# Kernel optimization log

Hardware: AMD Instinct MI355X
Metric: run time of the kernel (lower is better)

Reference implementation:

```python
import jax, jax.numpy as jnp
import numpy as np

DEPTH = 16
HID = 256
INP = 256
K = 2  # arity of the complete binary tree
TOTAL = (1 << (DEPTH + 1)) - 1  # 131071 nodes, level-order indexed


def setup_inputs() -> dict:
    key = jax.random.key(0)
    ks = jax.random.split(key, 14)
    s = 1.0 / np.sqrt(HID)
    inp = {
        "x": jax.random.normal(ks[0], (TOTAL, INP), jnp.float32),
        "Wi": jax.random.normal(ks[1], (HID, INP), jnp.float32) * s,
        "bi": jax.random.normal(ks[2], (HID,), jnp.float32) * s,
        "Wf": jax.random.normal(ks[3], (HID, INP), jnp.float32) * s,
        "bf": jax.random.normal(ks[4], (HID,), jnp.float32) * s,
        "Wo": jax.random.normal(ks[5], (HID, INP), jnp.float32) * s,
        "bo": jax.random.normal(ks[6], (HID,), jnp.float32) * s,
        "Wu": jax.random.normal(ks[7], (HID, INP), jnp.float32) * s,
        "bu": jax.random.normal(ks[8], (HID,), jnp.float32) * s,
        "Ui": jax.random.normal(ks[9], (HID, HID), jnp.float32) * s,
        "Uo": jax.random.normal(ks[10], (HID, HID), jnp.float32) * s,
        "Uu": jax.random.normal(ks[11], (HID, HID), jnp.float32) * s,
        "Wfk": jax.random.normal(ks[12], (K, HID, HID), jnp.float32) * s,
        "depth": DEPTH,
    }
    return inp


def reference(x, Wi, bi, Wf, bf, Wo, bo, Wu, bu, Ui, Uo, Uu, Wfk, depth):
    sig = jax.nn.sigmoid
    H = Ui.shape[0]
    # leaf level: leaf_forward (no recurrent terms)
    start, n = (1 << depth) - 1, 1 << depth
    xs = x[start:start + n]                      # [n, INP]
    i = sig(xs @ Wi.T + bi)
    o = sig(xs @ Wo.T + bo)
    u = jnp.tanh(xs @ Wu.T + bu)
    c = i * u
    h = o * jnp.tanh(c)
    # internal levels, bottom-up
    for d in range(depth - 1, -1, -1):
        start, n = (1 << d) - 1, 1 << d
        xs = x[start:start + n]                  # [n, INP]
        hc = h.reshape(n, K, H)                  # children h (level-order)
        cc = c.reshape(n, K, H)                  # children c
        Hs = hc.sum(axis=1)                      # sum over children, [n, H]
        i = sig(xs @ Wi.T + bi + Hs @ Ui.T)
        o = sig(xs @ Wo.T + bo + Hs @ Uo.T)
        u = jnp.tanh(xs @ Wu.T + bu + Hs @ Uu.T)
        # per-child-position forget gate; original applies wf{k} to the SUM of all children h
        fx = xs @ Wf.T + bf                      # [n, H]
        ukfh = jnp.einsum('ni,koi->nko', Hs, Wfk)  # [n, K, H]
        f = sig(fx[:, None, :] + ukfh)
        c = i * u + (f * cc).sum(axis=1)
        h = o * jnp.tanh(c)
    return jnp.stack([h, c])  # [2, 1, H]: root (h, c)
```

## Files before the change

### kernel.cpp

```cpp
#include <hip/hip_runtime.h>
#include <math.h>


#define LEAF_N 65536

typedef __attribute__((ext_vector_type(8))) short bf16x8;
typedef __attribute__((ext_vector_type(4))) float f32x4;

__device__ __forceinline__ float sigf(float x) { return 1.0f / (1.0f + expf(-x)); }

__device__ __forceinline__ unsigned short f2bf(float f) {
    union { float f; unsigned u; } v; v.f = f;
    unsigned r = v.u + 0x7fffu + ((v.u >> 16) & 1u);
    return (unsigned short)(r >> 16);
}

__host__ __device__ __forceinline__ size_t zoffD(int d) {
    return (d >= 4) ? (size_t)(65536 - (2 << d)) * 512
                    : (size_t)65536 * 512 + (size_t)(3 - d) * 8192;
}

__global__ __launch_bounds__(256) void pack_weights(
    const float* __restrict__ Wi, const float* __restrict__ bi,
    const float* __restrict__ Wf, const float* __restrict__ bf,
    const float* __restrict__ Wo, const float* __restrict__ bo,
    const float* __restrict__ Wu, const float* __restrict__ bu,
    const float* __restrict__ Ui, const float* __restrict__ Uo,
    const float* __restrict__ Uu, const float* __restrict__ Wfk,
    unsigned short* __restrict__ Wpk, unsigned short* __restrict__ WpkL,
    float* __restrict__ bbig, float* __restrict__ bleaf)
{
    int idx = blockIdx.x * 256 + threadIdx.x;
    const int NWB = 1280 * 512;
    const int NWL = 768 * 256;
    if (idx < NWB) {
        int j = idx & 7, l = (idx >> 3) & 63, kc = (idx >> 9) & 15, nt = idx >> 13;
        int row = nt * 16 + (l & 15);
        int k = kc * 32 + ((l >> 4) << 3) + j;
        int g = row >> 8, rr = row & 255;
        float v;
        if (k < 256) {
            const float* W = (g == 0) ? Wi : (g == 1) ? Wo : (g == 2) ? Wu : Wf;
            v = W[rr * 256 + k];
        } else {
            int kk = k - 256;
            v = (g == 0) ? Ui[rr * 256 + kk]
              : (g == 1) ? Uo[rr * 256 + kk]
              : (g == 2) ? Uu[rr * 256 + kk]
              : (g == 3) ? Wfk[rr * 256 + kk]
                         : Wfk[65536 + rr * 256 + kk];
        }
        Wpk[idx] = f2bf(v);
    } else if (idx < NWB + NWL) {
        int q = idx - NWB;
        int j = q & 7, l = (q >> 3) & 63, kc = (q >> 9) & 7, nt = q >> 12;
        int row = nt * 16 + (l & 15);
        int k = kc * 32 + ((l >> 4) << 3) + j;
        int g = row >> 8, rr = row & 255;
        const float* W = (g == 0) ? Wi : (g == 1) ? Wo : Wu;
        WpkL[q] = f2bf(W[rr * 256 + k]);
    } else if (idx < NWB + NWL + 1280) {
        int r = idx - NWB - NWL;
        int g = r >> 8, rr = r & 255;
        bbig[r] = (g == 0) ? bi[rr] : (g == 1) ? bo[rr] : (g == 2) ? bu[rr] : bf[rr];
    } else if (idx < NWB + NWL + 1280 + 768) {
        int r = idx - NWB - NWL - 1280;
        int g = r >> 8, rr = r & 255;
        bleaf[r] = (g == 0) ? bi[rr] : (g == 1) ? bo[rr] : bu[rr];
    }
}

__global__ __launch_bounds__(256) void cvt_all(
    const float* __restrict__ x, unsigned short* __restrict__ Zbuf,
    unsigned short* __restrict__ Xpk)
{
    int idx = blockIdx.x * 256 + threadIdx.x;
    if (idx >= 131071 * 32) return;
    int row = idx >> 5, k8 = idx & 31;
    const float* s = x + (size_t)row * 256 + k8 * 8;
    unsigned short r[8];
#pragma unroll
    for (int i = 0; i < 8; i++) r[i] = f2bf(s[i]);
    int kc = k8 >> 2;
    if (row < 65535) {
        int d = 31 - __clz(row + 1);
        int jn = row - ((1 << d) - 1);
        int l = (jn & 15) + ((k8 & 3) << 4);
        size_t dst = zoffD(d) + ((size_t)((jn >> 4) * 16 + kc) * 64 + l) * 8;
        *(uint4*)(Zbuf + dst) = *(uint4*)r;
    } else {
        int jn = row - 65535;
        int l = (jn & 15) + ((k8 & 3) << 4);
        size_t dst = ((size_t)((jn >> 4) * 8 + kc) * 64 + l) * 8;
        *(uint4*)(Xpk + dst) = *(uint4*)r;
    }
}

template<int NG, int KCN>
__global__ __launch_bounds__(512, 2) void fused_level(
    const unsigned short* __restrict__ Zpk, const unsigned short* __restrict__ Wpk,
    const float* __restrict__ bias, const float* __restrict__ csrc,
    float* __restrict__ c_out, unsigned short* __restrict__ zparent,
    int leaf_flag)
{
    const int tid = threadIdx.x, wave = tid >> 6, lane = tid & 63;
    const int bm = blockIdx.x * 32;
    const int cc = lane & 15, rq = (lane >> 4) * 4;

    f32x4 acc[2][2 * NG] = {};

    const unsigned short* aB = Zpk + ((size_t)(bm >> 4) * KCN * 64 + lane) * 8;
    const unsigned short* bB = Wpk + ((size_t)(2 * wave) * KCN * 64 + lane) * 8;

    bf16x8 afX[2], bvX[2 * NG];
    bf16x8 afY[2], bvY[2 * NG];

#pragma unroll
    for (int i = 0; i < 2; ++i)
        afX[i] = *(const bf16x8*)(aB + (size_t)(i * KCN) * 512);
#pragma unroll
    for (int g = 0; g < NG; ++g)
#pragma unroll
        for (int t = 0; t < 2; ++t)
            bvX[g * 2 + t] = *(const bf16x8*)(bB + (size_t)((g * 16 + t) * KCN) * 512);

    auto do_mfma = [&](bf16x8 (&af)[2], bf16x8 (&bv)[2 * NG]) {
#pragma unroll
        for (int g = 0; g < NG; ++g)
#pragma unroll
            for (int t = 0; t < 2; ++t)
#pragma unroll
                for (int i = 0; i < 2; ++i)
                    acc[i][g * 2 + t] = __builtin_amdgcn_mfma_f32_16x16x32_bf16(
                        af[i], bv[g * 2 + t], acc[i][g * 2 + t], 0, 0, 0);
    };

#pragma unroll
    for (int kc = 0; kc < KCN; kc += 2) {
#pragma unroll
        for (int i = 0; i < 2; ++i)
            afY[i] = *(const bf16x8*)(aB + (size_t)(i * KCN + kc + 1) * 512);
#pragma unroll
        for (int g = 0; g < NG; ++g)
#pragma unroll
            for (int t = 0; t < 2; ++t)
                bvY[g * 2 + t] = *(const bf16x8*)(bB + (size_t)((g * 16 + t) * KCN + kc + 1) * 512);
        do_mfma(afX, bvX);
        if (kc + 2 < KCN) {
#pragma unroll
            for (int i = 0; i < 2; ++i)
                afX[i] = *(const bf16x8*)(aB + (size_t)(i * KCN + kc + 2) * 512);
#pragma unroll
            for (int g = 0; g < NG; ++g)
#pragma unroll
                for (int t = 0; t < 2; ++t)
                    bvX[g * 2 + t] = *(const bf16x8*)(bB + (size_t)((g * 16 + t) * KCN + kc + 2) * 512);
        }
        do_mfma(afY, bvY);
    }

#pragma unroll
    for (int t = 0; t < 2; ++t) {
        const int h = (2 * wave + t) * 16 + cc;
        const float bI = bias[h], bO = bias[256 + h], bU = bias[512 + h];
        float bF0 = 0.f, bF1 = 0.f;
        if constexpr (NG == 5) { bF0 = bias[768 + h]; bF1 = bias[1024 + h]; }
#pragma unroll
        for (int mt = 0; mt < 2; ++mt) {
            const int node0 = bm + mt * 16 + rq;
            float hv[4];
#pragma unroll
            for (int r = 0; r < 4; ++r) {
                const int node = node0 + r;
                float iv = sigf(acc[mt][0 + t][r] + bI);
                float ov = sigf(acc[mt][2 + t][r] + bO);
                float uv = tanhf(acc[mt][4 + t][r] + bU);
                float cv = iv * uv;
                if constexpr (NG == 5) {
                    float f0 = sigf(acc[mt][6 + t][r] + bF0);
                    float f1 = sigf(acc[mt][8 + t][r] + bF1);
                    cv += f0 * csrc[(size_t)(2 * node) * 256 + h]
                        + f1 * csrc[(size_t)(2 * node + 1) * 256 + h];
                }
                c_out[(size_t)node * 256 + h] = cv;
                hv[r] = ov * tanhf(cv);
            }
#pragma unroll
            for (int pr = 0; pr < 2; ++pr) {
                const int p = ((node0 + 2 * pr) >> 1);
                size_t a = ((size_t)((p >> 4) * 16 + 8 + (h >> 5)) * 64
                            + (p & 15) + (((h >> 3) & 3) << 4)) * 8 + (h & 7);
                zparent[a] = f2bf(hv[2 * pr] + hv[2 * pr + 1]);
            }
        }
    }
    (void)leaf_flag;
}

__global__ __launch_bounds__(64) void small_gemm(
    const unsigned short* __restrict__ Zpk, const unsigned short* __restrict__ Wpk,
    const float* __restrict__ bias, float* __restrict__ pre, int n)
{
    const int lane = threadIdx.x;
    const int q = blockIdx.x;
    const int nt0 = (q >> 2) * 16 + (q & 3) * 4;
    const int cc = lane & 15, rq = (lane >> 4) * 4;

    f32x4 acc[4] = {};
    const unsigned short* aB = Zpk + (size_t)lane * 8;
    const unsigned short* bB = Wpk + ((size_t)nt0 * 16 * 64 + lane) * 8;

    bf16x8 aX, bX[4], aY, bY[4];
    aX = *(const bf16x8*)(aB);
#pragma unroll
    for (int j = 0; j < 4; ++j)
        bX[j] = *(const bf16x8*)(bB + (size_t)(j * 16) * 512);

#pragma unroll
    for (int kc = 0; kc < 16; kc += 2) {
        aY = *(const bf16x8*)(aB + (size_t)(kc + 1) * 512);
#pragma unroll
        for (int j = 0; j < 4; ++j)
            bY[j] = *(const bf16x8*)(bB + (size_t)(j * 16 + kc + 1) * 512);
#pragma unroll
        for (int j = 0; j < 4; ++j)
            acc[j] = __builtin_amdgcn_mfma_f32_16x16x32_bf16(aX, bX[j], acc[j], 0, 0, 0);
        if (kc + 2 < 16) {
            aX = *(const bf16x8*)(aB + (size_t)(kc + 2) * 512);
#pragma unroll
            for (int j = 0; j < 4; ++j)
                bX[j] = *(const bf16x8*)(bB + (size_t)(j * 16 + kc + 2) * 512);
        }
#pragma unroll
        for (int j = 0; j < 4; ++j)
            acc[j] = __builtin_amdgcn_mfma_f32_16x16x32_bf16(aY, bY[j], acc[j], 0, 0, 0);
    }

#pragma unroll
    for (int j = 0; j < 4; ++j) {
        int coln = (nt0 + j) * 16 + cc;
        float bb = bias[coln];
#pragma unroll
        for (int r = 0; r < 4; ++r) {
            int row = rq + r;
            if (row < n) pre[(size_t)row * 1280 + coln] = acc[j][r] + bb;
        }
    }
}

__global__ __launch_bounds__(256) void epi_small(
    const float* __restrict__ pre, const float* __restrict__ csrc,
    float* __restrict__ c_out, unsigned short* __restrict__ zparent,
    float* __restrict__ root_out, int npairs)
{
    int idx = blockIdx.x * 256 + threadIdx.x;
    if (root_out) {
        int h = idx;
        const float* p = pre;
        float c = sigf(p[h]) * tanhf(p[512 + h])
                + sigf(p[768 + h]) * csrc[h]
                + sigf(p[1024 + h]) * csrc[256 + h];
        root_out[h] = sigf(p[256 + h]) * tanhf(c);
        root_out[256 + h] = c;
        return;
    }
    if (idx >= npairs * 256) return;
    int pI = idx >> 8, h = idx & 255;
    int n0 = 2 * pI;
    const float* p0 = pre + (size_t)n0 * 1280;
    const float* p1 = p0 + 1280;
    float c0 = sigf(p0[h]) * tanhf(p0[512 + h])
             + sigf(p0[768 + h]) * csrc[(size_t)(2 * n0) * 256 + h]
             + sigf(p0[1024 + h]) * csrc[(size_t)(2 * n0 + 1) * 256 + h];
    float c1 = sigf(p1[h]) * tanhf(p1[512 + h])
             + sigf(p1[768 + h]) * csrc[(size_t)(2 * n0 + 2) * 256 + h]
             + sigf(p1[1024 + h]) * csrc[(size_t)(2 * n0 + 3) * 256 + h];
    float h0 = sigf(p0[256 + h]) * tanhf(c0);
    float h1 = sigf(p1[256 + h]) * tanhf(c1);
    c_out[(size_t)n0 * 256 + h] = c0;
    c_out[(size_t)(n0 + 1) * 256 + h] = c1;
    size_t a = ((size_t)((pI >> 4) * 16 + 8 + (h >> 5)) * 64
                + (pI & 15) + (((h >> 3) & 3) << 4)) * 8 + (h & 7);
    zparent[a] = f2bf(h0 + h1);
}

extern "C" void kernel_launch(void* const* d_in, const int* in_sizes, int n_in,
                              void* d_out, int out_size, void* d_ws, size_t ws_size,
                              hipStream_t stream)
{
    const float* x   = (const float*)d_in[0];
    const float* Wi  = (const float*)d_in[1];
    const float* bi  = (const float*)d_in[2];
    const float* Wf  = (const float*)d_in[3];
    const float* bf  = (const float*)d_in[4];
    const float* Wo  = (const float*)d_in[5];
    const float* bo  = (const float*)d_in[6];
    const float* Wu  = (const float*)d_in[7];
    const float* bu  = (const float*)d_in[8];
    const float* Ui  = (const float*)d_in[9];
    const float* Uo  = (const float*)d_in[10];
    const float* Uu  = (const float*)d_in[11];
    const float* Wfk = (const float*)d_in[12];
    float* out = (float*)d_out;
    char* ws   = (char*)d_ws;
    (void)ws_size; (void)in_sizes; (void)n_in; (void)out_size;

    size_t off = 0;
    unsigned short* Wpk  = (unsigned short*)(ws + off); off += (size_t)1280 * 512 * 2;
    unsigned short* WpkL = (unsigned short*)(ws + off); off += (size_t)768 * 256 * 2;
    float* bbig  = (float*)(ws + off); off += 1280 * 4;
    float* bleaf = (float*)(ws + off); off += 768 * 4 + 192;
    unsigned short* Xpk  = (unsigned short*)(ws + off); off += (size_t)65536 * 256 * 2;
    unsigned short* Zbuf = (unsigned short*)(ws + off); off += ((size_t)65536 * 512 + 32768) * 2;
    float* cA = (float*)(ws + off); off += (size_t)65536 * 256 * 4;
    float* cB = (float*)(ws + off); off += (size_t)32768 * 256 * 4;
    float* pre_small = (float*)(ws + off); off += (size_t)16 * 1280 * 4;

    pack_weights<<<3336, 256, 0, stream>>>(Wi, bi, Wf, bf, Wo, bo, Wu, bu,
                                           Ui, Uo, Uu, Wfk, Wpk, WpkL, bbig, bleaf);
    cvt_all<<<16385, 256, 0, stream>>>(x, Zbuf, Xpk);

    fused_level<3, 8><<<LEAF_N / 32, 512, 0, stream>>>(
        Xpk, WpkL, bleaf, nullptr, cA, Zbuf + zoffD(15), 1);

    for (int d = 15; d >= 5; d--) {
        float* csrc = (d & 1) ? cA : cB;
        float* cdst = (d & 1) ? cB : cA;
        fused_level<5, 16><<<1 << (d - 5), 512, 0, stream>>>(
            Zbuf + zoffD(d), Wpk, bbig, csrc, cdst, Zbuf + zoffD(d - 1), 0);
    }

    for (int d = 4; d >= 1; d--) {
        int n = 1 << d;
        float* csrc = (d & 1) ? cA : cB;
        float* cdst = (d & 1) ? cB : cA;
        small_gemm<<<20, 64, 0, stream>>>(Zbuf + zoffD(d), Wpk, bbig, pre_small, n);
        epi_small<<<n / 2, 256, 0, stream>>>(pre_small, csrc, cdst,
                                             Zbuf + zoffD(d - 1), nullptr, n / 2);
    }

    small_gemm<<<20, 64, 0, stream>>>(Zbuf + zoffD(0), Wpk, bbig, pre_small, 1);
    epi_small<<<1, 256, 0, stream>>>(pre_small, cB, nullptr, nullptr, out, 0);
}
```

Baseline: 963.0 us.

## Split fused level kernel into LDS-tiled gate GEMM and separate combine kernel

```diff
diff --git a/kernel.cpp b/kernel.cpp
--- a/kernel.cpp
+++ b/kernel.cpp
@@ -6,18 +6,25 @@
 
 typedef __attribute__((ext_vector_type(8))) short bf16x8;
 typedef __attribute__((ext_vector_type(4))) float f32x4;
+typedef unsigned short u16;
 
 __device__ __forceinline__ float sigf(float x) { return 1.0f / (1.0f + expf(-x)); }
 
-__device__ __forceinline__ unsigned short f2bf(float f) {
+__device__ __forceinline__ u16 f2bf(float f) {
     union { float f; unsigned u; } v; v.f = f;
     unsigned r = v.u + 0x7fffu + ((v.u >> 16) & 1u);
-    return (unsigned short)(r >> 16);
+    return (u16)(r >> 16);
 }
 
 __host__ __device__ __forceinline__ size_t zoffD(int d) {
     return (d >= 4) ? (size_t)(65536 - (2 << d)) * 512
                     : (size_t)65536 * 512 + (size_t)(3 - d) * 8192;
+}
+
+__device__ __forceinline__ void gld_lds16(const u16* g, u16* s) {
+    __builtin_amdgcn_global_load_lds(
+        (const __attribute__((address_space(1))) void*)g,
+        (__attribute__((address_space(3))) void*)s, 16, 0, 0);
 }
 
 __global__ __launch_bounds__(256) void pack_weights(
@@ -27,7 +34,7 @@
     const float* __restrict__ Wu, const float* __restrict__ bu,
     const float* __restrict__ Ui, const float* __restrict__ Uo,
     const float* __restrict__ Uu, const float* __restrict__ Wfk,
-    unsigned short* __restrict__ Wpk, unsigned short* __restrict__ WpkL,
+    u16* __restrict__ Wpk, u16* __restrict__ WpkL,
     float* __restrict__ bbig, float* __restrict__ bleaf)
 {
     int idx = blockIdx.x * 256 + threadIdx.x;
@@ -71,14 +78,13 @@
 }
 
 __global__ __launch_bounds__(256) void cvt_all(
-    const float* __restrict__ x, unsigned short* __restrict__ Zbuf,
-    unsigned short* __restrict__ Xpk)
+    const float* __restrict__ x, u16* __restrict__ Zbuf, u16* __restrict__ Xpk)
 {
     int idx = blockIdx.x * 256 + threadIdx.x;
     if (idx >= 131071 * 32) return;
     int row = idx >> 5, k8 = idx & 31;
     const float* s = x + (size_t)row * 256 + k8 * 8;
-    unsigned short r[8];
+    u16 r[8];
 #pragma unroll
     for (int i = 0; i < 8; i++) r[i] = f2bf(s[i]);
     int kc = k8 >> 2;
@@ -96,109 +102,112 @@
     }
 }
 
-template<int NG, int KCN>
-__global__ __launch_bounds__(512, 2) void fused_level(
-    const unsigned short* __restrict__ Zpk, const unsigned short* __restrict__ Wpk,
+template<int KCN>
+__global__ __launch_bounds__(256) void gate_gemm(
+    const u16* __restrict__ Zpk, const u16* __restrict__ Wpk,
     const float* __restrict__ bias, const float* __restrict__ csrc,
-    float* __restrict__ c_out, unsigned short* __restrict__ zparent,
-    int leaf_flag)
-{
+    _Float16* __restrict__ Ghalf, float* __restrict__ Gfc, int n)
+{
+    __shared__ u16 As[16 * 512];
+    __shared__ u16 Bs[16 * 512];
     const int tid = threadIdx.x, wave = tid >> 6, lane = tid & 63;
-    const int bm = blockIdx.x * 32;
+    const int bm = blockIdx.x * 128, bn = blockIdx.y;
+    const int wm = wave >> 1, wn = wave & 1;
     const int cc = lane & 15, rq = (lane >> 4) * 4;
 
-    f32x4 acc[2][2 * NG] = {};
-
-    const unsigned short* aB = Zpk + ((size_t)(bm >> 4) * KCN * 64 + lane) * 8;
-    const unsigned short* bB = Wpk + ((size_t)(2 * wave) * KCN * 64 + lane) * 8;
-
-    bf16x8 afX[2], bvX[2 * NG];
-    bf16x8 afY[2], bvY[2 * NG];
-
-#pragma unroll
-    for (int i = 0; i < 2; ++i)
-        afX[i] = *(const bf16x8*)(aB + (size_t)(i * KCN) * 512);
-#pragma unroll
-    for (int g = 0; g < NG; ++g)
-#pragma unroll
-        for (int t = 0; t < 2; ++t)
-            bvX[g * 2 + t] = *(const bf16x8*)(bB + (size_t)((g * 16 + t) * KCN) * 512);
-
-    auto do_mfma = [&](bf16x8 (&af)[2], bf16x8 (&bv)[2 * NG]) {
-#pragma unroll
-        for (int g = 0; g < NG; ++g)
-#pragma unroll
-            for (int t = 0; t < 2; ++t)
-#pragma unroll
-                for (int i = 0; i < 2; ++i)
-                    acc[i][g * 2 + t] = __builtin_amdgcn_mfma_f32_16x16x32_bf16(
-                        af[i], bv[g * 2 + t], acc[i][g * 2 + t], 0, 0, 0);
-    };
-
-#pragma unroll
-    for (int kc = 0; kc < KCN; kc += 2) {
-#pragma unroll
-        for (int i = 0; i < 2; ++i)
-            afY[i] = *(const bf16x8*)(aB + (size_t)(i * KCN + kc + 1) * 512);
-#pragma unroll
-        for (int g = 0; g < NG; ++g)
-#pragma unroll
-            for (int t = 0; t < 2; ++t)
-                bvY[g * 2 + t] = *(const bf16x8*)(bB + (size_t)((g * 16 + t) * KCN + kc + 1) * 512);
-        do_mfma(afX, bvX);
-        if (kc + 2 < KCN) {
-#pragma unroll
-            for (int i = 0; i < 2; ++i)
-                afX[i] = *(const bf16x8*)(aB + (size_t)(i * KCN + kc + 2) * 512);
-#pragma unroll
-            for (int g = 0; g < NG; ++g)
-#pragma unroll
-                for (int t = 0; t < 2; ++t)
-                    bvX[g * 2 + t] = *(const bf16x8*)(bB + (size_t)((g * 16 + t) * KCN + kc + 2) * 512);
-        }
-        do_mfma(afY, bvY);
-    }
-
-#pragma unroll
-    for (int t = 0; t < 2; ++t) {
-        const int h = (2 * wave + t) * 16 + cc;
-        const float bI = bias[h], bO = bias[256 + h], bU = bias[512 + h];
-        float bF0 = 0.f, bF1 = 0.f;
-        if constexpr (NG == 5) { bF0 = bias[768 + h]; bF1 = bias[1024 + h]; }
-#pragma unroll
-        for (int mt = 0; mt < 2; ++mt) {
-            const int node0 = bm + mt * 16 + rq;
-            float hv[4];
+    f32x4 acc[4][4] = {};
+    const u16* Ag = Zpk + (size_t)(bm >> 4) * KCN * 512;
+    const u16* Bg = Wpk + (size_t)(bn * 8) * KCN * 512;
+
+    for (int ch = 0; ch < KCN / 2; ++ch) {
+        const int kc0 = ch * 2;
+#pragma unroll
+        for (int q = 0; q < 8; ++q) {
+            int fid = wave * 8 + q;
+            if (fid < 16) {
+                int rt = fid >> 1, kc = fid & 1;
+                gld_lds16(Ag + ((size_t)rt * KCN + kc0 + kc) * 512 + lane * 8,
+                          As + fid * 512);
+            } else {
+                int f2 = fid - 16, nt = f2 >> 1, kc = f2 & 1;
+                gld_lds16(Bg + ((size_t)nt * KCN + kc0 + kc) * 512 + lane * 8,
+                          Bs + f2 * 512);
+            }
+        }
+        __syncthreads();
+#pragma unroll
+        for (int kc = 0; kc < 2; ++kc) {
+            bf16x8 af[4], bfr[4];
+#pragma unroll
+            for (int i = 0; i < 4; ++i)
+                af[i] = *(const bf16x8*)(As + ((wm * 4 + i) * 2 + kc) * 512 + lane * 8);
+#pragma unroll
+            for (int j = 0; j < 4; ++j)
+                bfr[j] = *(const bf16x8*)(Bs + ((wn * 4 + j) * 2 + kc) * 512 + lane * 8);
+#pragma unroll
+            for (int i = 0; i < 4; ++i)
+#pragma unroll
+                for (int j = 0; j < 4; ++j)
+                    acc[i][j] = __builtin_amdgcn_mfma_f32_16x16x32_bf16(
+                        af[i], bfr[j], acc[i][j], 0, 0, 0);
+        }
+        __syncthreads();
+    }
+
+    const int g = bn >> 1;
+#pragma unroll
+    for (int j = 0; j < 4; ++j) {
+        const int col = bn * 128 + (wn * 4 + j) * 16 + cc;
+        const float bb = bias[col];
+#pragma unroll
+        for (int i = 0; i < 4; ++i) {
+            const int row0 = bm + (wm * 4 + i) * 16 + rq;
 #pragma unroll
             for (int r = 0; r < 4; ++r) {
-                const int node = node0 + r;
-                float iv = sigf(acc[mt][0 + t][r] + bI);
-                float ov = sigf(acc[mt][2 + t][r] + bO);
-                float uv = tanhf(acc[mt][4 + t][r] + bU);
-                float cv = iv * uv;
-                if constexpr (NG == 5) {
-                    float f0 = sigf(acc[mt][6 + t][r] + bF0);
-                    float f1 = sigf(acc[mt][8 + t][r] + bF1);
-                    cv += f0 * csrc[(size_t)(2 * node) * 256 + h]
-                        + f1 * csrc[(size_t)(2 * node + 1) * 256 + h];
+                const int row = row0 + r;
+                if (row >= n) continue;
+                const float v = acc[i][j][r] + bb;
+                if (g == 2) {
+                    Ghalf[(size_t)row * 768 + col] = (_Float16)tanhf(v);
+                } else if (g < 2) {
+                    Ghalf[(size_t)row * 768 + col] = (_Float16)sigf(v);
+                } else {
+                    const float cch = csrc[(size_t)(2 * row + (g - 3)) * 256
+                                           + (col - g * 256)];
+                    Gfc[(size_t)row * 512 + (col - 768)] = sigf(v) * cch;
                 }
-                c_out[(size_t)node * 256 + h] = cv;
-                hv[r] = ov * tanhf(cv);
             }
-#pragma unroll
-            for (int pr = 0; pr < 2; ++pr) {
-                const int p = ((node0 + 2 * pr) >> 1);
-                size_t a = ((size_t)((p >> 4) * 16 + 8 + (h >> 5)) * 64
-                            + (p & 15) + (((h >> 3) & 3) << 4)) * 8 + (h & 7);
-                zparent[a] = f2bf(hv[2 * pr] + hv[2 * pr + 1]);
-            }
-        }
-    }
-    (void)leaf_flag;
+        }
+    }
+}
+
+template<bool LEAF>
+__global__ __launch_bounds__(256) void combine(
+    const _Float16* __restrict__ Ghalf, const float* __restrict__ Gfc,
+    float* __restrict__ cdst, u16* __restrict__ zparent)
+{
+    const int p = blockIdx.x, h = threadIdx.x;
+    const size_t n0 = (size_t)2 * p;
+    const _Float16* G0 = Ghalf + n0 * 768;
+    const _Float16* G1 = G0 + 768;
+    float i0 = (float)G0[h], o0 = (float)G0[256 + h], u0 = (float)G0[512 + h];
+    float i1 = (float)G1[h], o1 = (float)G1[256 + h], u1 = (float)G1[512 + h];
+    float c0 = i0 * u0, c1 = i1 * u1;
+    if (!LEAF) {
+        const float* F = Gfc + n0 * 512;
+        c0 += F[h] + F[256 + h];
+        c1 += F[512 + h] + F[768 + h];
+    }
+    float h0 = o0 * tanhf(c0), h1 = o1 * tanhf(c1);
+    cdst[n0 * 256 + h] = c0;
+    cdst[n0 * 256 + 256 + h] = c1;
+    size_t a = (((size_t)(p >> 4) * 16 + 8 + (h >> 5)) * 64
+                + (p & 15) + (((h >> 3) & 3) << 4)) * 8 + (h & 7);
+    zparent[a] = f2bf(h0 + h1);
 }
 
 __global__ __launch_bounds__(64) void small_gemm(
-    const unsigned short* __restrict__ Zpk, const unsigned short* __restrict__ Wpk,
+    const u16* __restrict__ Zpk, const u16* __restrict__ Wpk,
     const float* __restrict__ bias, float* __restrict__ pre, int n)
 {
     const int lane = threadIdx.x;
@@ -207,8 +216,8 @@
     const int cc = lane & 15, rq = (lane >> 4) * 4;
 
     f32x4 acc[4] = {};
-    const unsigned short* aB = Zpk + (size_t)lane * 8;
-    const unsigned short* bB = Wpk + ((size_t)nt0 * 16 * 64 + lane) * 8;
+    const u16* aB = Zpk + (size_t)lane * 8;
+    const u16* bB = Wpk + ((size_t)nt0 * 16 * 64 + lane) * 8;
 
     bf16x8 aX, bX[4], aY, bY[4];
     aX = *(const bf16x8*)(aB);
@@ -250,7 +259,7 @@
 
 __global__ __launch_bounds__(256) void epi_small(
     const float* __restrict__ pre, const float* __restrict__ csrc,
-    float* __restrict__ c_out, unsigned short* __restrict__ zparent,
+    float* __restrict__ c_out, u16* __restrict__ zparent,
     float* __restrict__ root_out, int npairs)
 {
     int idx = blockIdx.x * 256 + threadIdx.x;
@@ -306,28 +315,35 @@
     (void)ws_size; (void)in_sizes; (void)n_in; (void)out_size;
 
     size_t off = 0;
-    unsigned short* Wpk  = (unsigned short*)(ws + off); off += (size_t)1280 * 512 * 2;
-    unsigned short* WpkL = (unsigned short*)(ws + off); off += (size_t)768 * 256 * 2;
+    u16* Wpk  = (u16*)(ws + off); off += (size_t)1280 * 512 * 2;
+    u16* WpkL = (u16*)(ws + off); off += (size_t)768 * 256 * 2;
     float* bbig  = (float*)(ws + off); off += 1280 * 4;
     float* bleaf = (float*)(ws + off); off += 768 * 4 + 192;
-    unsigned short* Xpk  = (unsigned short*)(ws + off); off += (size_t)65536 * 256 * 2;
-    unsigned short* Zbuf = (unsigned short*)(ws + off); off += ((size_t)65536 * 512 + 32768) * 2;
+    u16* Xpk  = (u16*)(ws + off); off += (size_t)65536 * 256 * 2;
+    u16* Zbuf = (u16*)(ws + off); off += ((size_t)65536 * 512 + 32768) * 2;
     float* cA = (float*)(ws + off); off += (size_t)65536 * 256 * 4;
     float* cB = (float*)(ws + off); off += (size_t)32768 * 256 * 4;
     float* pre_small = (float*)(ws + off); off += (size_t)16 * 1280 * 4;
+    _Float16* Ghalf = (_Float16*)(ws + off); off += (size_t)65536 * 768 * 2;
+    float* Gfc = (float*)(ws + off); off += (size_t)32768 * 512 * 4;
 
     pack_weights<<<3336, 256, 0, stream>>>(Wi, bi, Wf, bf, Wo, bo, Wu, bu,
                                            Ui, Uo, Uu, Wfk, Wpk, WpkL, bbig, bleaf);
     cvt_all<<<16385, 256, 0, stream>>>(x, Zbuf, Xpk);
 
-    fused_level<3, 8><<<LEAF_N / 32, 512, 0, stream>>>(
-        Xpk, WpkL, bleaf, nullptr, cA, Zbuf + zoffD(15), 1);
+    gate_gemm<8><<<dim3(LEAF_N / 128, 6), 256, 0, stream>>>(
+        Xpk, WpkL, bleaf, nullptr, Ghalf, nullptr, LEAF_N);
+    combine<true><<<LEAF_N / 2, 256, 0, stream>>>(
+        Ghalf, nullptr, cA, Zbuf + zoffD(15));
 
     for (int d = 15; d >= 5; d--) {
+        int n = 1 << d;
         float* csrc = (d & 1) ? cA : cB;
         float* cdst = (d & 1) ? cB : cA;
-        fused_level<5, 16><<<1 << (d - 5), 512, 0, stream>>>(
-            Zbuf + zoffD(d), Wpk, bbig, csrc, cdst, Zbuf + zoffD(d - 1), 0);
+        gate_gemm<16><<<dim3((n + 127) / 128, 10), 256, 0, stream>>>(
+            Zbuf + zoffD(d), Wpk, bbig, csrc, Ghalf, Gfc, n);
+        combine<false><<<n / 2, 256, 0, stream>>>(
+            Ghalf, Gfc, cdst, Zbuf + zoffD(d - 1));
     }
 
     for (int d = 4; d >= 1; d--) {
```

Result: slower. 1.211 ms (+25.8%).
